# Kernel optimization log

Hardware: AMD Instinct MI355X
Metric: run time of the kernel (lower is better)

## Reference

```python
import jax, jax.numpy as jnp
import numpy as np

B, N, M, DIM, H, DH = 2, 2048, 2048, 512, 8, 64
INNER = H * DH  # 512


def setup_inputs() -> dict:
    key = jax.random.key(0)
    ks = jax.random.split(key, 9)
    s = 0.02
    return {
        "x": jax.random.normal(ks[0], (B, N, DIM), jnp.float32),
        "x1": jax.random.normal(ks[1], (B, M, DIM), jnp.float32),
        "attn_mat": jax.random.normal(ks[2], (B, H, N, M), jnp.float32),
        "dots_para": jax.random.uniform(ks[3], (1,), jnp.float32),
        "mat_para": jax.random.uniform(ks[4], (1,), jnp.float32),
        "W_qv": jax.random.normal(ks[5], (DIM, 2 * INNER), jnp.float32) * s,
        "W_k": jax.random.normal(ks[6], (DIM, INNER), jnp.float32) * s,
        "W_out": jax.random.normal(ks[7], (INNER, DIM), jnp.float32) * s,
        "b_out": jax.random.normal(ks[8], (DIM,), jnp.float32) * s,
    }


def _split_heads(t):
    # [b, n, h*d] -> [b, h, n, d]
    b, n, _ = t.shape
    return t.reshape(b, n, H, DH).transpose(0, 2, 1, 3)


def reference(x, x1, attn_mat, dots_para, mat_para, W_qv, W_k, W_out, b_out):
    scale = DH ** -0.5
    qv = x @ W_qv                      # [b, n, 2*inner]
    q, v = jnp.split(qv, 2, axis=-1)
    q = _split_heads(q)                # [b, h, n, d]
    v = _split_heads(v)                # [b, h, n, d]
    k = _split_heads(x1 @ W_k)         # [b, h, m, d]
    dots = jnp.einsum("bhnd,bhmd->bhnm", q, k) * scale
    dots = dots * dots_para + attn_mat * mat_para
    attn = jax.nn.softmax(dots, axis=-1)
    out = jnp.einsum("bhnm,bhmd->bhnd", attn, v)
    out = out.transpose(0, 2, 1, 3).reshape(x.shape[0], x.shape[1], INNER)
    return out @ W_out + b_out
```

## Files before the change

### kernel.cpp

```cpp
#include <hip/hip_runtime.h>

#define NB 2048
#define MB 2048
#define SPLITS 4
#define MSP (MB / SPLITS)

typedef __attribute__((ext_vector_type(8))) short short8;
typedef __attribute__((ext_vector_type(4))) float floatx4;

__device__ __forceinline__ unsigned short f2bf(float f) {
    union { float f; unsigned int u; } v; v.f = f;
    unsigned int r = (v.u + 0x7FFFu + ((v.u >> 16) & 1u)) >> 16;
    return (unsigned short)r;
}

__device__ __forceinline__ int swz(int row, int k) {
    return (row << 6) + ((((k >> 3) ^ (row & 7))) << 3) + (k & 7);
}
__device__ __forceinline__ int vswz(int row, int k) {
    return (row << 6) + ((((k >> 3) ^ (row & 7) ^ ((row >> 3) & 7))) << 3) + (k & 7);
}

__device__ __forceinline__ void gload16(const unsigned short* g, short* l) {
    __builtin_amdgcn_global_load_lds(
        (const __attribute__((address_space(1))) void*)g,
        (__attribute__((address_space(3))) void*)l, 16, 0, 0);
}

__launch_bounds__(256)
__global__ void prep(const float* __restrict__ x, const float* __restrict__ x1,
                     const float* __restrict__ Wqv, const float* __restrict__ Wk,
                     const float* __restrict__ Wout,
                     unsigned short* __restrict__ xb, unsigned short* __restrict__ x1b,
                     unsigned short* __restrict__ Wqvt, unsigned short* __restrict__ Wkt,
                     unsigned short* __restrict__ Woutt) {
    __shared__ float t[64][65];
    const int bid = blockIdx.x, tid = threadIdx.x;
    if (bid < 2048) {
        const float* in = bid < 1024 ? x : x1;
        unsigned short* out = bid < 1024 ? xb : x1b;
        size_t off = ((size_t)(bid & 1023) * 256 + tid) * 8;
        float4 d0 = *(const float4*)(in + off);
        float4 d1 = *(const float4*)(in + off + 4);
        uint4 o;
        o.x = (unsigned int)f2bf(d0.x) | ((unsigned int)f2bf(d0.y) << 16);
        o.y = (unsigned int)f2bf(d0.z) | ((unsigned int)f2bf(d0.w) << 16);
        o.z = (unsigned int)f2bf(d1.x) | ((unsigned int)f2bf(d1.y) << 16);
        o.w = (unsigned int)f2bf(d1.z) | ((unsigned int)f2bf(d1.w) << 16);
        *(uint4*)(out + off) = o;
        return;
    }
    int tb = bid - 2048;
    const float* W; unsigned short* Wt; int N;
    if (tb < 128)      { W = Wqv;  Wt = Wqvt;  N = 1024; }
    else if (tb < 192) { tb -= 128; W = Wk;   Wt = Wkt;   N = 512; }
    else               { tb -= 192; W = Wout; Wt = Woutt; N = 512; }
    const int k0 = (tb & 7) * 64, n0 = (tb >> 3) * 64;
#pragma unroll
    for (int p = 0; p < 4; p++) {
        int idx = p * 256 + tid;
        int kr = idx >> 4, c4 = (idx & 15) << 2;
        float4 d = *(const float4*)(W + (size_t)(k0 + kr) * N + n0 + c4);
        t[kr][c4 + 0] = d.x; t[kr][c4 + 1] = d.y; t[kr][c4 + 2] = d.z; t[kr][c4 + 3] = d.w;
    }
    __syncthreads();
#pragma unroll
    for (int p = 0; p < 4; p++) {
        int idx = p * 256 + tid;
        int nr = idx >> 4, k4 = (idx & 15) << 2;
        uint2 o;
        o.x = (unsigned int)f2bf(t[k4 + 0][nr]) | ((unsigned int)f2bf(t[k4 + 1][nr]) << 16);
        o.y = (unsigned int)f2bf(t[k4 + 2][nr]) | ((unsigned int)f2bf(t[k4 + 3][nr]) << 16);
        *(uint2*)(Wt + (size_t)(n0 + nr) * 512 + k0 + k4) = o;
    }
}

template <int OUT_BF16>
__device__ __forceinline__ void gemm_body(const unsigned short* __restrict__ A,
                                          const unsigned short* __restrict__ Bt,
                                          const float* __restrict__ bias,
                                          void* __restrict__ Cp, int Nc, int m0, int n0,
                                          short* Al, short* Bl) {
    const int tid = threadIdx.x;
    const int w = tid >> 6, lane = tid & 63;
    const int quad = lane >> 4, c16 = lane & 15;
    const int wm = (w >> 1) * 64, wn = (w & 1) * 32;

    floatx4 acc[4][2];
#pragma unroll
    for (int i = 0; i < 4; i++)
#pragma unroll
        for (int j = 0; j < 2; j++) acc[i][j] = floatx4{0.f, 0.f, 0.f, 0.f};

    const unsigned short* Ap = A + (size_t)m0 * 512;
    const unsigned short* Bp = Bt + (size_t)n0 * 512;

    auto stage = [&](int bufi, int kk) {
#pragma unroll
        for (int p = 0; p < 4; p++) {
            int idx = p * 256 + tid;
            int row = idx >> 3, c = idx & 7;
            gload16(Ap + (size_t)row * 512 + kk + ((c ^ (row & 7)) << 3),
                    Al + bufi * 8192 + idx * 8);
        }
#pragma unroll
        for (int p = 0; p < 2; p++) {
            int idx = p * 256 + tid;
            int row = idx >> 3, c = idx & 7;
            gload16(Bp + (size_t)row * 512 + kk + ((c ^ (row & 7)) << 3),
                    Bl + bufi * 4096 + idx * 8);
        }
    };

    stage(0, 0);
    __syncthreads();

    for (int ks = 0; ks < 8; ks++) {
        const int buf = ks & 1;
        if (ks < 7) stage(buf ^ 1, (ks + 1) * 64);
#pragma unroll
        for (int kc = 0; kc < 2; kc++) {
            short8 af[4], bf[2];
#pragma unroll
            for (int mt = 0; mt < 4; mt++)
                af[mt] = *(const short8*)&Al[buf * 8192 + swz(wm + mt * 16 + c16, kc * 32 + quad * 8)];
#pragma unroll
            for (int nt = 0; nt < 2; nt++)
                bf[nt] = *(const short8*)&Bl[buf * 4096 + swz(wn + nt * 16 + c16, kc * 32 + quad * 8)];
#pragma unroll
            for (int mt = 0; mt < 4; mt++)
#pragma unroll
                for (int nt = 0; nt < 2; nt++)
                    acc[mt][nt] = __builtin_amdgcn_mfma_f32_16x16x32_bf16(af[mt], bf[nt], acc[mt][nt], 0, 0, 0);
        }
        __syncthreads();
    }
#pragma unroll
    for (int mt = 0; mt < 4; mt++)
#pragma unroll
        for (int nt = 0; nt < 2; nt++)
#pragma unroll
            for (int r = 0; r < 4; r++) {
                int row = m0 + wm + mt * 16 + quad * 4 + r;
                int col = n0 + wn + nt * 16 + c16;
                float v = acc[mt][nt][r];
                if (OUT_BF16) {
                    ((unsigned short*)Cp)[(size_t)row * Nc + col] = f2bf(v);
                } else {
                    ((float*)Cp)[(size_t)row * Nc + col] = v + bias[col];
                }
            }
}

__launch_bounds__(256)
__global__ void gemm_qvk(const unsigned short* __restrict__ xb, const unsigned short* __restrict__ x1b,
                         const unsigned short* __restrict__ Wqvt, const unsigned short* __restrict__ Wkt,
                         unsigned short* __restrict__ qvbf, unsigned short* __restrict__ kbf) {
    __shared__ short Al[2 * 128 * 64];
    __shared__ short Bl[2 * 64 * 64];
    int bid = blockIdx.x;
    if (bid < 512) {
        gemm_body<1>(xb, Wqvt, nullptr, qvbf, 1024, (bid & 31) * 128, (bid >> 5) * 64, Al, Bl);
    } else {
        bid -= 512;
        gemm_body<1>(x1b, Wkt, nullptr, kbf, 512, (bid & 31) * 128, (bid >> 5) * 64, Al, Bl);
    }
}

__launch_bounds__(256)
__global__ void gemm_out(const unsigned short* __restrict__ A, const unsigned short* __restrict__ Bt,
                         const float* __restrict__ bias, float* __restrict__ C) {
    __shared__ short Al[2 * 128 * 64];
    __shared__ short Bl[2 * 64 * 64];
    gemm_body<0>(A, Bt, bias, C, 512, blockIdx.x * 128, blockIdx.y * 64, Al, Bl);
}

__launch_bounds__(256)
__global__ void flash_attn(const unsigned short* __restrict__ qv,
                           const unsigned short* __restrict__ kb,
                           const float* __restrict__ attn_mat,
                           const float* __restrict__ dots_para,
                           const float* __restrict__ mat_para,
                           float* __restrict__ Opart,
                           float* __restrict__ lpart) {
    __shared__ short QP[4][32 * 64];
    __shared__ short Ks[2][64 * 64];
    __shared__ short Vs[2][64 * 64];

    const int tid = threadIdx.x, w = tid >> 6, lane = tid & 63;
    const int quad = lane >> 4, c16 = lane & 15;
    const int q0 = blockIdx.x * 128;
    const int bh = blockIdx.y;
    const int sp = blockIdx.z;
    const int b = bh >> 3, h = bh & 7;
    const int ms = sp * MSP;

    const float log2e = 1.4426950408889634f;
    const float mp = mat_para[0] * log2e;
    const float sdp = dots_para[0] * 0.125f * log2e;

    short* QPf = (short*)QP;
    const int sr = tid >> 3, sc = tid & 7;

#pragma unroll
    for (int p = 0; p < 4; p++) {
        int idx = p * 256 + tid;
        int r = idx >> 3, c = idx & 7;
        gload16(qv + (size_t)(b * NB + q0 + r) * 1024 + h * 64 + ((c ^ (r & 7)) << 3),
                QPf + idx * 8);
    }

    auto gloadK = [&](int bufi, int m) {
#pragma unroll
        for (int p = 0; p < 2; p++) {
            int idx = p * 256 + tid;
            int row = idx >> 3, c = idx & 7;
            gload16(kb + (size_t)(b * MB + m + row) * 512 + h * 64 + ((c ^ (row & 7)) << 3),
                    &Ks[bufi][idx * 8]);
        }
    };

    uint4 vreg[2];
    auto loadV = [&](int m) {
#pragma unroll
        for (int p = 0; p < 2; p++) {
            int r = p * 32 + sr;
            vreg[p] = *(const uint4*)(qv + (size_t)(b * NB + m + r) * 1024 + 512 + h * 64 + sc * 8);
        }
    };
    auto storeV = [&](int bufi) {
#pragma unroll
        for (int p = 0; p < 2; p++) {
            int r = p * 32 + sr;
            uint4 d = vreg[p];
            Vs[bufi][vswz(sc * 8 + 0, r)] = (short)(d.x & 0xffff);
            Vs[bufi][vswz(sc * 8 + 1, r)] = (short)(d.x >> 16);
            Vs[bufi][vswz(sc * 8 + 2, r)] = (short)(d.y & 0xffff);
            Vs[bufi][vswz(sc * 8 + 3, r)] = (short)(d.y >> 16);
            Vs[bufi][vswz(sc * 8 + 4, r)] = (short)(d.z & 0xffff);
            Vs[bufi][vswz(sc * 8 + 5, r)] = (short)(d.z >> 16);
            Vs[bufi][vswz(sc * 8 + 6, r)] = (short)(d.w & 0xffff);
            Vs[bufi][vswz(sc * 8 + 7, r)] = (short)(d.w >> 16);
        }
    };
    const float* amp = attn_mat + ((size_t)bh * NB + q0 + w * 32 + quad * 4) * MB + c16;
    float amr[2][4][4];
    auto loadAM = [&](int m0_) {
#pragma unroll
        for (int at = 0; at < 2; at++)
#pragma unroll
            for (int r = 0; r < 4; r++)
#pragma unroll
                for (int t = 0; t < 4; t++)
                    amr[at][t][r] = amp[(size_t)(at * 16 + r) * MB + m0_ + t * 16];
    };

    gloadK(0, ms);
    loadV(ms);
    loadAM(ms);
    __syncthreads();
    short8 qf[2][2];
#pragma unroll
    for (int at = 0; at < 2; at++)
#pragma unroll
        for (int kc = 0; kc < 2; kc++)
            qf[at][kc] = *(const short8*)&QPf[swz(w * 32 + at * 16 + c16, kc * 32 + quad * 8)];
    short* Pw = &QPf[w * 2048];
    storeV(0);
    loadV(ms + 64);

    floatx4 O[2][4];
    float l[2][4];
#pragma unroll
    for (int at = 0; at < 2; at++)
#pragma unroll
        for (int i = 0; i < 4; i++) { O[at][i] = floatx4{0.f, 0.f, 0.f, 0.f}; l[at][i] = 0.f; }

    for (int it = 0; it < MSP / 64; it++) {
        const int m0 = ms + it * 64;
        const int buf = it & 1, nbuf = buf ^ 1;
        __syncthreads();
        int mn1 = m0 + 64;  if (mn1 >= ms + MSP) mn1 = ms;
        int mn2 = m0 + 128; if (mn2 >= ms + MSP) mn2 = ms;
        gloadK(nbuf, mn1);
        storeV(nbuf);
        loadV(mn2);

        floatx4 S[2][4];
        __builtin_amdgcn_s_setprio(1);
#pragma unroll
        for (int t = 0; t < 4; t++) {
            short8 kf0 = *(const short8*)&Ks[buf][swz(t * 16 + c16, quad * 8)];
            short8 kf1 = *(const short8*)&Ks[buf][swz(t * 16 + c16, 32 + quad * 8)];
#pragma unroll
            for (int at = 0; at < 2; at++) {
                floatx4 s = floatx4{0.f, 0.f, 0.f, 0.f};
                s = __builtin_amdgcn_mfma_f32_16x16x32_bf16(qf[at][0], kf0, s, 0, 0, 0);
                s = __builtin_amdgcn_mfma_f32_16x16x32_bf16(qf[at][1], kf1, s, 0, 0, 0);
                S[at][t] = s;
            }
        }
        __builtin_amdgcn_s_setprio(0);

#pragma unroll
        for (int at = 0; at < 2; at++)
#pragma unroll
            for (int t = 0; t < 4; t++) {
                float p0 = exp2f(fmaf(S[at][t][0], sdp, amr[at][t][0] * mp));
                float p1 = exp2f(fmaf(S[at][t][1], sdp, amr[at][t][1] * mp));
                float p2 = exp2f(fmaf(S[at][t][2], sdp, amr[at][t][2] * mp));
                float p3 = exp2f(fmaf(S[at][t][3], sdp, amr[at][t][3] * mp));
                l[at][0] += p0; l[at][1] += p1; l[at][2] += p2; l[at][3] += p3;
                unsigned int w01, w23;
                asm("v_cvt_pk_bf16_f32 %0, %1, %2" : "=v"(w01) : "v"(p0), "v"(p1));
                asm("v_cvt_pk_bf16_f32 %0, %1, %2" : "=v"(w23) : "v"(p2), "v"(p3));
                int br = at * 16 + quad * 4;
                Pw[swz(br + 0, t * 16 + c16)] = (short)(w01 & 0xffff);
                Pw[swz(br + 1, t * 16 + c16)] = (short)(w01 >> 16);
                Pw[swz(br + 2, t * 16 + c16)] = (short)(w23 & 0xffff);
                Pw[swz(br + 3, t * 16 + c16)] = (short)(w23 >> 16);
            }
        loadAM(mn1);
        __threadfence_block();

        short8 pf[2][2];
#pragma unroll
        for (int at = 0; at < 2; at++)
#pragma unroll
            for (int kc = 0; kc < 2; kc++)
                pf[at][kc] = *(const short8*)&Pw[swz(at * 16 + c16, kc * 32 + quad * 8)];
        __builtin_amdgcn_s_setprio(1);
#pragma unroll
        for (int dt = 0; dt < 4; dt++) {
            short8 vf0 = *(const short8*)&Vs[buf][vswz(dt * 16 + c16, quad * 8)];
            short8 vf1 = *(const short8*)&Vs[buf][vswz(dt * 16 + c16, 32 + quad * 8)];
#pragma unroll
            for (int at = 0; at < 2; at++) {
                O[at][dt] = __builtin_amdgcn_mfma_f32_16x16x32_bf16(pf[at][0], vf0, O[at][dt], 0, 0, 0);
                O[at][dt] = __builtin_amdgcn_mfma_f32_16x16x32_bf16(pf[at][1], vf1, O[at][dt], 0, 0, 0);
            }
        }
        __builtin_amdgcn_s_setprio(0);
    }

#pragma unroll
    for (int at = 0; at < 2; at++) {
#pragma unroll
        for (int r = 0; r < 4; r++) {
            float s = l[at][r];
            s += __shfl_xor(s, 1);
            s += __shfl_xor(s, 2);
            s += __shfl_xor(s, 4);
            s += __shfl_xor(s, 8);
            l[at][r] = s;
        }
        if (c16 == 0) {
#pragma unroll
            for (int r = 0; r < 4; r++)
                lpart[(size_t)(sp * 16 + bh) * NB + q0 + w * 32 + at * 16 + quad * 4 + r] = l[at][r];
        }
#pragma unroll
        for (int dt = 0; dt < 4; dt++)
#pragma unroll
            for (int r = 0; r < 4; r++) {
                size_t row = (size_t)sp * 4096 + b * NB + q0 + w * 32 + at * 16 + quad * 4 + r;
                Opart[row * 512 + h * 64 + dt * 16 + c16] = O[at][dt][r];
            }
    }
}

__launch_bounds__(256)
__global__ void combine_splits(const float* __restrict__ Opart, const float* __restrict__ lpart,
                               unsigned short* __restrict__ ao) {
    int idx = blockIdx.x * 256 + threadIdx.x;
    int row = idx >> 7;
    int col = (idx & 127) << 2;
    int b = row >> 11, n = row & 2047, h = col >> 6;
    float ls = 0.f;
    float4 o = {0.f, 0.f, 0.f, 0.f};
#pragma unroll
    for (int sp = 0; sp < SPLITS; sp++) {
        ls += lpart[(size_t)(sp * 16 + b * 8 + h) * NB + n];
        float4 os = *(const float4*)(Opart + ((size_t)sp * 4096 + row) * 512 + col);
        o.x += os.x; o.y += os.y; o.z += os.z; o.w += os.w;
    }
    float rinv = 1.0f / ls;
    uint2 pk;
    pk.x = (unsigned int)f2bf(o.x * rinv) | ((unsigned int)f2bf(o.y * rinv) << 16);
    pk.y = (unsigned int)f2bf(o.z * rinv) | ((unsigned int)f2bf(o.w * rinv) << 16);
    *(uint2*)(ao + (size_t)row * 512 + col) = pk;
}

extern "C" void kernel_launch(void* const* d_in, const int* in_sizes, int n_in,
                              void* d_out, int out_size, void* d_ws, size_t ws_size,
                              hipStream_t stream) {
    const float* x         = (const float*)d_in[0];
    const float* x1        = (const float*)d_in[1];
    const float* attn_mat  = (const float*)d_in[2];
    const float* dots_para = (const float*)d_in[3];
    const float* mat_para  = (const float*)d_in[4];
    const float* W_qv      = (const float*)d_in[5];
    const float* W_k       = (const float*)d_in[6];
    const float* W_out     = (const float*)d_in[7];
    const float* b_out     = (const float*)d_in[8];
    float* out = (float*)d_out;

    unsigned short* xb    = (unsigned short*)d_ws;
    unsigned short* x1b   = xb    + (size_t)4096 * 512;
    unsigned short* qvbf  = x1b   + (size_t)4096 * 512;
    unsigned short* kbf   = qvbf  + (size_t)4096 * 1024;
    unsigned short* aobf  = kbf   + (size_t)4096 * 512;
    unsigned short* Wqvt  = aobf  + (size_t)4096 * 512;
    unsigned short* Wkt   = Wqvt  + (size_t)1024 * 512;
    unsigned short* Woutt = Wkt   + (size_t)512 * 512;
    float*          Opart = (float*)(Woutt + (size_t)512 * 512);
    float*          lpart = Opart + (size_t)SPLITS * 4096 * 512;

    dim3 blk(256);
    prep<<<2304, blk, 0, stream>>>(x, x1, W_qv, W_k, W_out, xb, x1b, Wqvt, Wkt, Woutt);
    gemm_qvk<<<768, blk, 0, stream>>>(xb, x1b, Wqvt, Wkt, qvbf, kbf);
    flash_attn<<<dim3(16, 16, SPLITS), blk, 0, stream>>>(qvbf, kbf, attn_mat, dots_para, mat_para, Opart, lpart);
    combine_splits<<<2048, blk, 0, stream>>>(Opart, lpart, aobf);
    gemm_out<<<dim3(32, 8), blk, 0, stream>>>(aobf, Woutt, b_out, out);
}
```

Baseline: 432.8 us.

## Merge split-K attention into one 512-thread block with in-LDS combine

```diff
diff --git a/kernel.cpp b/kernel.cpp
--- a/kernel.cpp
+++ b/kernel.cpp
@@ -2,8 +2,6 @@
 
 #define NB 2048
 #define MB 2048
-#define SPLITS 4
-#define MSP (MB / SPLITS)
 
 typedef __attribute__((ext_vector_type(8))) short short8;
 typedef __attribute__((ext_vector_type(4))) float floatx4;
@@ -175,48 +173,49 @@
     gemm_body<0>(A, Bt, bias, C, 512, blockIdx.x * 128, blockIdx.y * 64, Al, Bl);
 }
 
-__launch_bounds__(256)
+__launch_bounds__(512, 2)
 __global__ void flash_attn(const unsigned short* __restrict__ qv,
                            const unsigned short* __restrict__ kb,
                            const float* __restrict__ attn_mat,
                            const float* __restrict__ dots_para,
                            const float* __restrict__ mat_para,
-                           float* __restrict__ Opart,
-                           float* __restrict__ lpart) {
-    __shared__ short QP[4][32 * 64];
-    __shared__ short Ks[2][64 * 64];
-    __shared__ short Vs[2][64 * 64];
+                           unsigned short* __restrict__ ao) {
+    __shared__ short Qs[128 * 64];
+    __shared__ short Ps[8][32 * 64];
+    __shared__ short Ks[2][2][64 * 64];
+    __shared__ short Vs[2][2][64 * 64];
 
     const int tid = threadIdx.x, w = tid >> 6, lane = tid & 63;
+    const int st = w >> 2;
+    const int wq = w & 3;
     const int quad = lane >> 4, c16 = lane & 15;
     const int q0 = blockIdx.x * 128;
     const int bh = blockIdx.y;
-    const int sp = blockIdx.z;
     const int b = bh >> 3, h = bh & 7;
-    const int ms = sp * MSP;
+    const int ms = st * 1024;
 
     const float log2e = 1.4426950408889634f;
     const float mp = mat_para[0] * log2e;
     const float sdp = dots_para[0] * 0.125f * log2e;
 
-    short* QPf = (short*)QP;
-    const int sr = tid >> 3, sc = tid & 7;
-
-#pragma unroll
-    for (int p = 0; p < 4; p++) {
-        int idx = p * 256 + tid;
+#pragma unroll
+    for (int p = 0; p < 2; p++) {
+        int idx = p * 512 + tid;
         int r = idx >> 3, c = idx & 7;
         gload16(qv + (size_t)(b * NB + q0 + r) * 1024 + h * 64 + ((c ^ (r & 7)) << 3),
-                QPf + idx * 8);
-    }
+                Qs + idx * 8);
+    }
+
+    const int gt = tid & 255;
+    const int sr = gt >> 3, sc = gt & 7;
 
     auto gloadK = [&](int bufi, int m) {
 #pragma unroll
         for (int p = 0; p < 2; p++) {
-            int idx = p * 256 + tid;
+            int idx = p * 256 + gt;
             int row = idx >> 3, c = idx & 7;
             gload16(kb + (size_t)(b * MB + m + row) * 512 + h * 64 + ((c ^ (row & 7)) << 3),
-                    &Ks[bufi][idx * 8]);
+                    &Ks[st][bufi][idx * 8]);
         }
     };
 
@@ -233,17 +232,18 @@
         for (int p = 0; p < 2; p++) {
             int r = p * 32 + sr;
             uint4 d = vreg[p];
-            Vs[bufi][vswz(sc * 8 + 0, r)] = (short)(d.x & 0xffff);
-            Vs[bufi][vswz(sc * 8 + 1, r)] = (short)(d.x >> 16);
-            Vs[bufi][vswz(sc * 8 + 2, r)] = (short)(d.y & 0xffff);
-            Vs[bufi][vswz(sc * 8 + 3, r)] = (short)(d.y >> 16);
-            Vs[bufi][vswz(sc * 8 + 4, r)] = (short)(d.z & 0xffff);
-            Vs[bufi][vswz(sc * 8 + 5, r)] = (short)(d.z >> 16);
-            Vs[bufi][vswz(sc * 8 + 6, r)] = (short)(d.w & 0xffff);
-            Vs[bufi][vswz(sc * 8 + 7, r)] = (short)(d.w >> 16);
+            short* V = &Vs[st][bufi][0];
+            V[vswz(sc * 8 + 0, r)] = (short)(d.x & 0xffff);
+            V[vswz(sc * 8 + 1, r)] = (short)(d.x >> 16);
+            V[vswz(sc * 8 + 2, r)] = (short)(d.y & 0xffff);
+            V[vswz(sc * 8 + 3, r)] = (short)(d.y >> 16);
+            V[vswz(sc * 8 + 4, r)] = (short)(d.z & 0xffff);
+            V[vswz(sc * 8 + 5, r)] = (short)(d.z >> 16);
+            V[vswz(sc * 8 + 6, r)] = (short)(d.w & 0xffff);
+            V[vswz(sc * 8 + 7, r)] = (short)(d.w >> 16);
         }
     };
-    const float* amp = attn_mat + ((size_t)bh * NB + q0 + w * 32 + quad * 4) * MB + c16;
+    const float* amp = attn_mat + ((size_t)bh * NB + q0 + wq * 32 + quad * 4) * MB + c16;
     float amr[2][4][4];
     auto loadAM = [&](int m0_) {
 #pragma unroll
@@ -264,8 +264,8 @@
     for (int at = 0; at < 2; at++)
 #pragma unroll
         for (int kc = 0; kc < 2; kc++)
-            qf[at][kc] = *(const short8*)&QPf[swz(w * 32 + at * 16 + c16, kc * 32 + quad * 8)];
-    short* Pw = &QPf[w * 2048];
+            qf[at][kc] = *(const short8*)&Qs[swz(wq * 32 + at * 16 + c16, kc * 32 + quad * 8)];
+    short* Pw = &Ps[w][0];
     storeV(0);
     loadV(ms + 64);
 
@@ -276,12 +276,12 @@
 #pragma unroll
         for (int i = 0; i < 4; i++) { O[at][i] = floatx4{0.f, 0.f, 0.f, 0.f}; l[at][i] = 0.f; }
 
-    for (int it = 0; it < MSP / 64; it++) {
+    for (int it = 0; it < 16; it++) {
         const int m0 = ms + it * 64;
         const int buf = it & 1, nbuf = buf ^ 1;
         __syncthreads();
-        int mn1 = m0 + 64;  if (mn1 >= ms + MSP) mn1 = ms;
-        int mn2 = m0 + 128; if (mn2 >= ms + MSP) mn2 = ms;
+        int mn1 = ms + ((it + 1) & 15) * 64;
+        int mn2 = ms + ((it + 2) & 15) * 64;
         gloadK(nbuf, mn1);
         storeV(nbuf);
         loadV(mn2);
@@ -290,8 +290,8 @@
         __builtin_amdgcn_s_setprio(1);
 #pragma unroll
         for (int t = 0; t < 4; t++) {
-            short8 kf0 = *(const short8*)&Ks[buf][swz(t * 16 + c16, quad * 8)];
-            short8 kf1 = *(const short8*)&Ks[buf][swz(t * 16 + c16, 32 + quad * 8)];
+            short8 kf0 = *(const short8*)&Ks[st][buf][swz(t * 16 + c16, quad * 8)];
+            short8 kf1 = *(const short8*)&Ks[st][buf][swz(t * 16 + c16, 32 + quad * 8)];
 #pragma unroll
             for (int at = 0; at < 2; at++) {
                 floatx4 s = floatx4{0.f, 0.f, 0.f, 0.f};
@@ -332,8 +332,8 @@
         __builtin_amdgcn_s_setprio(1);
 #pragma unroll
         for (int dt = 0; dt < 4; dt++) {
-            short8 vf0 = *(const short8*)&Vs[buf][vswz(dt * 16 + c16, quad * 8)];
-            short8 vf1 = *(const short8*)&Vs[buf][vswz(dt * 16 + c16, 32 + quad * 8)];
+            short8 vf0 = *(const short8*)&Vs[st][buf][vswz(dt * 16 + c16, quad * 8)];
+            short8 vf1 = *(const short8*)&Vs[st][buf][vswz(dt * 16 + c16, 32 + quad * 8)];
 #pragma unroll
             for (int at = 0; at < 2; at++) {
                 O[at][dt] = __builtin_amdgcn_mfma_f32_16x16x32_bf16(pf[at][0], vf0, O[at][dt], 0, 0, 0);
@@ -344,7 +344,7 @@
     }
 
 #pragma unroll
-    for (int at = 0; at < 2; at++) {
+    for (int at = 0; at < 2; at++)
 #pragma unroll
         for (int r = 0; r < 4; r++) {
             float s = l[at][r];
@@ -354,41 +354,43 @@
             s += __shfl_xor(s, 8);
             l[at][r] = s;
         }
-        if (c16 == 0) {
+
+    __syncthreads();
+    float* Of = (float*)&Ks[0][0][0];
+    float* lf = (float*)&Vs[0][0][0];
+    if (st == 1) {
+#pragma unroll
+        for (int at = 0; at < 2; at++) {
+#pragma unroll
+            for (int dt = 0; dt < 4; dt++)
+#pragma unroll
+                for (int r = 0; r < 4; r++)
+                    Of[(size_t)(wq * 32 + at * 16 + quad * 4 + r) * 64 + dt * 16 + c16] = O[at][dt][r];
+            if (c16 == 0)
+#pragma unroll
+                for (int r = 0; r < 4; r++)
+                    lf[wq * 32 + at * 16 + quad * 4 + r] = l[at][r];
+        }
+    }
+    __syncthreads();
+    if (st == 0) {
+#pragma unroll
+        for (int at = 0; at < 2; at++) {
+            float rinv[4];
 #pragma unroll
             for (int r = 0; r < 4; r++)
-                lpart[(size_t)(sp * 16 + bh) * NB + q0 + w * 32 + at * 16 + quad * 4 + r] = l[at][r];
-        }
-#pragma unroll
-        for (int dt = 0; dt < 4; dt++)
-#pragma unroll
-            for (int r = 0; r < 4; r++) {
-                size_t row = (size_t)sp * 4096 + b * NB + q0 + w * 32 + at * 16 + quad * 4 + r;
-                Opart[row * 512 + h * 64 + dt * 16 + c16] = O[at][dt][r];
-            }
-    }
-}
-
-__launch_bounds__(256)
-__global__ void combine_splits(const float* __restrict__ Opart, const float* __restrict__ lpart,
-                               unsigned short* __restrict__ ao) {
-    int idx = blockIdx.x * 256 + threadIdx.x;
-    int row = idx >> 7;
-    int col = (idx & 127) << 2;
-    int b = row >> 11, n = row & 2047, h = col >> 6;
-    float ls = 0.f;
-    float4 o = {0.f, 0.f, 0.f, 0.f};
-#pragma unroll
-    for (int sp = 0; sp < SPLITS; sp++) {
-        ls += lpart[(size_t)(sp * 16 + b * 8 + h) * NB + n];
-        float4 os = *(const float4*)(Opart + ((size_t)sp * 4096 + row) * 512 + col);
-        o.x += os.x; o.y += os.y; o.z += os.z; o.w += os.w;
-    }
-    float rinv = 1.0f / ls;
-    uint2 pk;
-    pk.x = (unsigned int)f2bf(o.x * rinv) | ((unsigned int)f2bf(o.y * rinv) << 16);
-    pk.y = (unsigned int)f2bf(o.z * rinv) | ((unsigned int)f2bf(o.w * rinv) << 16);
-    *(uint2*)(ao + (size_t)row * 512 + col) = pk;
+                rinv[r] = 1.0f / (l[at][r] + lf[wq * 32 + at * 16 + quad * 4 + r]);
+#pragma unroll
+            for (int dt = 0; dt < 4; dt++)
+#pragma unroll
+                for (int r = 0; r < 4; r++) {
+                    int row = wq * 32 + at * 16 + quad * 4 + r;
+                    float osum = O[at][dt][r] + Of[(size_t)row * 64 + dt * 16 + c16];
+                    ao[(size_t)(b * NB + q0 + row) * 512 + h * 64 + dt * 16 + c16] =
+                        f2bf(osum * rinv[at == 0 ? r : r]);
+                }
+        }
+    }
 }
 
 extern "C" void kernel_launch(void* const* d_in, const int* in_sizes, int n_in,
@@ -413,13 +415,10 @@
     unsigned short* Wqvt  = aobf  + (size_t)4096 * 512;
     unsigned short* Wkt   = Wqvt  + (size_t)1024 * 512;
     unsigned short* Woutt = Wkt   + (size_t)512 * 512;
-    float*          Opart = (float*)(Woutt + (size_t)512 * 512);
-    float*          lpart = Opart + (size_t)SPLITS * 4096 * 512;
 
     dim3 blk(256);
     prep<<<2304, blk, 0, stream>>>(x, x1, W_qv, W_k, W_out, xb, x1b, Wqvt, Wkt, Woutt);
     gemm_qvk<<<768, blk, 0, stream>>>(xb, x1b, Wqvt, Wkt, qvbf, kbf);
-    flash_attn<<<dim3(16, 16, SPLITS), blk, 0, stream>>>(qvbf, kbf, attn_mat, dots_para, mat_para, Opart, lpart);
-    combine_splits<<<2048, blk, 0, stream>>>(Opart, lpart, aobf);
+    flash_attn<<<dim3(16, 16), dim3(512), 0, stream>>>(qvbf, kbf, attn_mat, dots_para, mat_para, aobf);
     gemm_out<<<dim3(32, 8), blk, 0, stream>>>(aobf, Woutt, b_out, out);
 }
```

Measured after the change: 444.2 us. 1.03x slower.
